# Optimization experiments

Measured on AMD Instinct MI355X. Metric: run time of the kernel, lower is better.

Reference implementation:

```python
import jax, jax.numpy as jnp
import numpy as np

N = 50000          # nodes
E = 800000         # edges (before self-loops)
G = 64             # graphs in batch
VOCAB = 10000
EMB = 62
HEADS = 4
C = 64             # per-head channels
NUM_CLASSES = 10
NEG_SLOPE = 0.2


def setup_inputs() -> dict:
    key = jax.random.key(0)
    ks = jax.random.split(key, 24)
    inp = {}
    inp['x_ids'] = jax.random.randint(ks[0], (N,), 0, VOCAB)
    inp['degrees'] = jax.random.uniform(ks[1], (N, 2), dtype=jnp.float32)
    inp['edge_src'] = jax.random.randint(ks[2], (E,), 0, N)
    inp['edge_dst'] = jax.random.randint(ks[3], (E,), 0, N)
    inp['batch'] = jnp.sort(jax.random.randint(ks[4], (N,), 0, G))
    # parameters
    inp['emb'] = jax.random.normal(ks[5], (VOCAB, EMB), dtype=jnp.float32)
    d_in = EMB + 2  # 64
    s = lambda f: 1.0 / np.sqrt(f)
    inp['W1'] = jax.random.normal(ks[6], (HEADS * C, d_in), dtype=jnp.float32) * s(d_in)
    inp['as1'] = jax.random.normal(ks[7], (HEADS, C), dtype=jnp.float32) * s(C)
    inp['ad1'] = jax.random.normal(ks[8], (HEADS, C), dtype=jnp.float32) * s(C)
    inp['b1'] = jnp.zeros((HEADS * C,), dtype=jnp.float32)
    inp['W2'] = jax.random.normal(ks[9], (HEADS * C, HEADS * C), dtype=jnp.float32) * s(HEADS * C)
    inp['as2'] = jax.random.normal(ks[10], (HEADS, C), dtype=jnp.float32) * s(C)
    inp['ad2'] = jax.random.normal(ks[11], (HEADS, C), dtype=jnp.float32) * s(C)
    inp['b2'] = jnp.zeros((HEADS * C,), dtype=jnp.float32)
    inp['W3'] = jax.random.normal(ks[12], (1 * C, HEADS * C), dtype=jnp.float32) * s(HEADS * C)
    inp['as3'] = jax.random.normal(ks[13], (1, C), dtype=jnp.float32) * s(C)
    inp['ad3'] = jax.random.normal(ks[14], (1, C), dtype=jnp.float32) * s(C)
    inp['b3'] = jnp.zeros((C,), dtype=jnp.float32)
    inp['linW'] = jax.random.normal(ks[15], (NUM_CLASSES, C), dtype=jnp.float32) * s(C)
    inp['linb'] = jnp.zeros((NUM_CLASSES,), dtype=jnp.float32)
    return inp


def gat_conv(x, src, dst, W, att_src, att_dst, bias, heads, out_ch, concat):
    n = x.shape[0]
    h = (x @ W.T).reshape(n, heads, out_ch)              # [N,H,C]
    a_src = jnp.sum(h * att_src, axis=-1)                # [N,H]
    a_dst = jnp.sum(h * att_dst, axis=-1)                # [N,H]
    e = jax.nn.leaky_relu(a_src[src] + a_dst[dst], NEG_SLOPE)  # [E,H]
    # segmented softmax over incoming edges of each dst node
    emax = jax.ops.segment_max(e, dst, num_segments=n)
    ex = jnp.exp(e - emax[dst])
    denom = jax.ops.segment_sum(ex, dst, num_segments=n)
    alpha = ex / (denom[dst] + 1e-16)                    # [E,H]
    msg = h[src] * alpha[:, :, None]                     # [E,H,C]
    out = jax.ops.segment_sum(msg, dst, num_segments=n)  # [N,H,C]
    out = out.reshape(n, heads * out_ch) if concat else out.mean(axis=1)
    return out + bias


def reference(x_ids, degrees, edge_src, edge_dst, batch, emb,
              W1, as1, ad1, b1, W2, as2, ad2, b2, W3, as3, ad3, b3, linW, linb):
    n = x_ids.shape[0]
    # add self-loops (PyG GATConv default)
    loop = jnp.arange(n)
    src = jnp.concatenate([edge_src, loop])
    dst = jnp.concatenate([edge_dst, loop])
    x = jnp.concatenate([emb[x_ids], degrees], axis=1)   # [N, EMB+2]
    x = jax.nn.relu(gat_conv(x, src, dst, W1, as1, ad1, b1, HEADS, C, True))
    x = jax.nn.relu(gat_conv(x, src, dst, W2, as2, ad2, b2, HEADS, C, True))
    x = jax.nn.relu(gat_conv(x, src, dst, W3, as3, ad3, b3, 1, C, False))
    # global mean pool over graphs
    sums = jax.ops.segment_sum(x, batch, num_segments=G)                    # [G,C]
    cnts = jax.ops.segment_sum(jnp.ones((n,), x.dtype), batch, num_segments=G)
    pooled = sums / jnp.maximum(cnts, 1.0)[:, None]
    return pooled @ linW.T + linb                         # [G, num_classes]
```

## Files before the change

### kernel.cpp

```cpp
#include <hip/hip_runtime.h>
#include <hip/hip_bf16.h>
#include <cstdint>

#define NEG_SLOPE 0.2f

typedef __bf16 bf16x8 __attribute__((ext_vector_type(8)));
typedef float  f32x4  __attribute__((ext_vector_type(4)));

__device__ __forceinline__ unsigned short f2bf(float f) {
    unsigned int u = __float_as_uint(f);
    u += 0x7fffu + ((u >> 16) & 1u);
    return (unsigned short)(u >> 16);
}
__device__ __forceinline__ float bf2f(unsigned short u) {
    return __uint_as_float((unsigned int)u << 16);
}
__device__ __forceinline__ void fma2(float2& a, float ex, unsigned int u) {
    a.x = fmaf(ex, __uint_as_float(u << 16),         a.x);
    a.y = fmaf(ex, __uint_as_float(u & 0xffff0000u), a.y);
}

__global__ void prep_kernel(const float* __restrict__ W1, int n1,
                            const float* __restrict__ W2, int n2,
                            const float* __restrict__ W3, int n3,
                            unsigned short* __restrict__ w1b, unsigned short* __restrict__ w2b,
                            unsigned short* __restrict__ w3b,
                            const int* __restrict__ ids, const float* __restrict__ degs,
                            const float* __restrict__ emb, unsigned short* __restrict__ x,
                            int* __restrict__ cnt, int* __restrict__ bucket,
                            int* __restrict__ n_over,
                            const int* __restrict__ batch, int* __restrict__ gcnt,
                            int Nn, int G, int bW, int bX)
{
    int b = blockIdx.x;
    if (b < bW) {
        int i = b * 256 + threadIdx.x;
        if (i < n1) w1b[i] = f2bf(W1[i]);
        int j = i - n1;
        if (j >= 0 && j < n2) w2b[j] = f2bf(W2[j]);
        int k = j - n2;
        if (k >= 0 && k < n3) w3b[k] = f2bf(W3[k]);
    } else if (b < bX) {
        int node = (b - bW) * 4 + (threadIdx.x >> 6);
        int lane = threadIdx.x & 63;
        if (node < Nn) {
            int id = ids[node];
            float v;
            if (lane < 62) v = emb[(size_t)id * 62 + lane];
            else           v = degs[node * 2 + (lane - 62)];
            x[(size_t)node * 64 + lane] = f2bf(v);
            if (lane == 0) {
                cnt[node] = 1;
                bucket[(size_t)node * 64] = node;
            }
        }
    } else {
        int g = threadIdx.x;
        if (g < G) {
            int lo0 = 0, hi = Nn;
            while (lo0 < hi) { int mid = (lo0 + hi) >> 1; if (batch[mid] < g) lo0 = mid + 1; else hi = mid; }
            int lo1 = lo0; hi = Nn;
            while (lo1 < hi) { int mid = (lo1 + hi) >> 1; if (batch[mid] < g + 1) lo1 = mid + 1; else hi = mid; }
            gcnt[g] = lo1 - lo0;
        }
        if (threadIdx.x == 255) *n_over = 0;
    }
}

__global__ void gemm_scatter(const unsigned short* __restrict__ X, const unsigned short* __restrict__ Wb,
                             unsigned short* __restrict__ Hout,
                             const float* __restrict__ aSrc, const float* __restrict__ aDst,
                             float* __restrict__ a_s, float* __restrict__ a_d,
                             int Nn, int K, int F, int gemmB,
                             const int* __restrict__ esrc, const int* __restrict__ edst,
                             int* __restrict__ cnt, int* __restrict__ bucket,
                             int* __restrict__ ovd, int* __restrict__ ovs, int* __restrict__ n_over,
                             int E0)
{
    if (blockIdx.x >= gemmB) {
        int base = (blockIdx.x - gemmB) * 1024 + threadIdx.x;
        int sv[4], dv[4], pv[4];
        bool ok[4];
#pragma unroll
        for (int k = 0; k < 4; ++k) {
            int e = base + k * 256;
            ok[k] = (e < E0);
            if (ok[k]) { sv[k] = esrc[e]; dv[k] = edst[e]; }
        }
#pragma unroll
        for (int k = 0; k < 4; ++k)
            if (ok[k]) pv[k] = atomicAdd(&cnt[dv[k]], 1);
#pragma unroll
        for (int k = 0; k < 4; ++k) {
            if (ok[k]) {
                if (pv[k] < 64) bucket[(size_t)dv[k] * 64 + pv[k]] = sv[k];
                else {
                    int o = atomicAdd(n_over, 1);
                    ovd[o] = dv[k]; ovs[o] = sv[k];
                }
            }
        }
        return;
    }

    int wid  = (blockIdx.x * blockDim.x + threadIdx.x) >> 6;
    int lane = threadIdx.x & 63;
    int mtiles = (Nn + 63) >> 6;
    int ftiles = F >> 6;
    if (wid >= mtiles * ftiles) return;
    int ft = wid % ftiles;
    int mt = wid / ftiles;
    int m0 = mt << 6, f0 = ft << 6;
    int r = lane & 15, g = lane >> 4, g4 = g << 2;

    const unsigned short* xrow[4];
#pragma unroll
    for (int ja = 0; ja < 4; ++ja) {
        int row = m0 + ja * 16 + r;
        if (row >= Nn) row = Nn - 1;
        xrow[ja] = X + (size_t)row * K + g * 8;
    }
    const unsigned short* wrow = Wb + (size_t)(f0 + r) * K + g * 8;
    const size_t wstep = (size_t)16 * K;

    f32x4 acc[4][4];
#pragma unroll
    for (int a = 0; a < 4; ++a)
#pragma unroll
        for (int b = 0; b < 4; ++b) acc[a][b] = f32x4{0.f, 0.f, 0.f, 0.f};

    for (int k0 = 0; k0 < K; k0 += 32) {
        bf16x8 av[4], bv[4];
#pragma unroll
        for (int ja = 0; ja < 4; ++ja) av[ja] = *reinterpret_cast<const bf16x8*>(xrow[ja] + k0);
#pragma unroll
        for (int jb = 0; jb < 4; ++jb) bv[jb] = *reinterpret_cast<const bf16x8*>(wrow + jb * wstep + k0);
#pragma unroll
        for (int ja = 0; ja < 4; ++ja)
#pragma unroll
            for (int jb = 0; jb < 4; ++jb)
                acc[ja][jb] = __builtin_amdgcn_mfma_f32_16x16x32_bf16(av[ja], bv[jb], acc[ja][jb], 0, 0, 0);
    }

#pragma unroll
    for (int ja = 0; ja < 4; ++ja)
#pragma unroll
        for (int q = 0; q < 4; ++q) {
            int row = m0 + ja * 16 + g4 + q;
            if (row < Nn) {
#pragma unroll
                for (int jb = 0; jb < 4; ++jb)
                    Hout[(size_t)row * F + f0 + jb * 16 + r] = f2bf(acc[ja][jb][q]);
            }
        }

    float ps[4][4], pd[4][4];
#pragma unroll
    for (int ja = 0; ja < 4; ++ja)
#pragma unroll
        for (int q = 0; q < 4; ++q) { ps[ja][q] = 0.f; pd[ja][q] = 0.f; }
#pragma unroll
    for (int jb = 0; jb < 4; ++jb) {
        float ws_ = aSrc[f0 + jb * 16 + r];
        float wd_ = aDst[f0 + jb * 16 + r];
#pragma unroll
        for (int ja = 0; ja < 4; ++ja)
#pragma unroll
            for (int q = 0; q < 4; ++q) {
                ps[ja][q] += acc[ja][jb][q] * ws_;
                pd[ja][q] += acc[ja][jb][q] * wd_;
            }
    }
#pragma unroll
    for (int off = 1; off < 16; off <<= 1)
#pragma unroll
        for (int ja = 0; ja < 4; ++ja)
#pragma unroll
            for (int q = 0; q < 4; ++q) {
                ps[ja][q] += __shfl_xor(ps[ja][q], off, 64);
                pd[ja][q] += __shfl_xor(pd[ja][q], off, 64);
            }
    if (r == 0) {
        int Hh = F >> 6;
#pragma unroll
        for (int ja = 0; ja < 4; ++ja)
#pragma unroll
            for (int q = 0; q < 4; ++q) {
                int n = m0 + ja * 16 + g4 + q;
                if (n < Nn) {
                    a_s[(size_t)n * Hh + ft] = ps[ja][q];
                    a_d[(size_t)n * Hh + ft] = pd[ja][q];
                }
            }
    }
}

__global__ void gemm_mfma(const unsigned short* __restrict__ X, const unsigned short* __restrict__ Wb,
                          unsigned short* __restrict__ Hout,
                          const float* __restrict__ aSrc, const float* __restrict__ aDst,
                          float* __restrict__ a_s, float* __restrict__ a_d,
                          int Nn, int K, int F)
{
    int wid  = (blockIdx.x * blockDim.x + threadIdx.x) >> 6;
    int lane = threadIdx.x & 63;
    int mtiles = (Nn + 63) >> 6;
    int ftiles = F >> 6;
    if (wid >= mtiles * ftiles) return;
    int ft = wid % ftiles;
    int mt = wid / ftiles;
    int m0 = mt << 6, f0 = ft << 6;
    int r = lane & 15, g = lane >> 4, g4 = g << 2;

    const unsigned short* xrow[4];
#pragma unroll
    for (int ja = 0; ja < 4; ++ja) {
        int row = m0 + ja * 16 + r;
        if (row >= Nn) row = Nn - 1;
        xrow[ja] = X + (size_t)row * K + g * 8;
    }
    const unsigned short* wrow = Wb + (size_t)(f0 + r) * K + g * 8;
    const size_t wstep = (size_t)16 * K;

    f32x4 acc[4][4];
#pragma unroll
    for (int a = 0; a < 4; ++a)
#pragma unroll
        for (int b = 0; b < 4; ++b) acc[a][b] = f32x4{0.f, 0.f, 0.f, 0.f};

    for (int k0 = 0; k0 < K; k0 += 32) {
        bf16x8 av[4], bv[4];
#pragma unroll
        for (int ja = 0; ja < 4; ++ja) av[ja] = *reinterpret_cast<const bf16x8*>(xrow[ja] + k0);
#pragma unroll
        for (int jb = 0; jb < 4; ++jb) bv[jb] = *reinterpret_cast<const bf16x8*>(wrow + jb * wstep + k0);
#pragma unroll
        for (int ja = 0; ja < 4; ++ja)
#pragma unroll
            for (int jb = 0; jb < 4; ++jb)
                acc[ja][jb] = __builtin_amdgcn_mfma_f32_16x16x32_bf16(av[ja], bv[jb], acc[ja][jb], 0, 0, 0);
    }

#pragma unroll
    for (int ja = 0; ja < 4; ++ja)
#pragma unroll
        for (int q = 0; q < 4; ++q) {
            int row = m0 + ja * 16 + g4 + q;
            if (row < Nn) {
#pragma unroll
                for (int jb = 0; jb < 4; ++jb)
                    Hout[(size_t)row * F + f0 + jb * 16 + r] = f2bf(acc[ja][jb][q]);
            }
        }

    float ps[4][4], pd[4][4];
#pragma unroll
    for (int ja = 0; ja < 4; ++ja)
#pragma unroll
        for (int q = 0; q < 4; ++q) { ps[ja][q] = 0.f; pd[ja][q] = 0.f; }
#pragma unroll
    for (int jb = 0; jb < 4; ++jb) {
        float ws_ = aSrc[f0 + jb * 16 + r];
        float wd_ = aDst[f0 + jb * 16 + r];
#pragma unroll
        for (int ja = 0; ja < 4; ++ja)
#pragma unroll
            for (int q = 0; q < 4; ++q) {
                ps[ja][q] += acc[ja][jb][q] * ws_;
                pd[ja][q] += acc[ja][jb][q] * wd_;
            }
    }
#pragma unroll
    for (int off = 1; off < 16; off <<= 1)
#pragma unroll
        for (int ja = 0; ja < 4; ++ja)
#pragma unroll
            for (int q = 0; q < 4; ++q) {
                ps[ja][q] += __shfl_xor(ps[ja][q], off, 64);
                pd[ja][q] += __shfl_xor(pd[ja][q], off, 64);
            }
    if (r == 0) {
        int Hh = F >> 6;
#pragma unroll
        for (int ja = 0; ja < 4; ++ja)
#pragma unroll
            for (int q = 0; q < 4; ++q) {
                int n = m0 + ja * 16 + g4 + q;
                if (n < Nn) {
                    a_s[(size_t)n * Hh + ft] = ps[ja][q];
                    a_d[(size_t)n * Hh + ft] = pd[ja][q];
                }
            }
    }
}

template<int H>
__global__ void aggregate_kernel(const unsigned short* __restrict__ Hb,
                                 const float* __restrict__ a_s, const float* __restrict__ a_d,
                                 const int* __restrict__ cnt, const int* __restrict__ bucket,
                                 const int* __restrict__ ovd, const int* __restrict__ ovs,
                                 const int* __restrict__ n_over,
                                 const float* __restrict__ bias,
                                 unsigned short* __restrict__ out, int Nn)
{
    constexpr int F = H * 64;
    constexpr int VEC = F / 64;
    __shared__ uint2 s_pk[4][64][H];
    int w = threadIdx.x >> 6;
    int node = blockIdx.x * 4 + w;
    int lane = threadIdx.x & 63;
    if (node >= Nn) return;
    int deg = cnt[node];

    float adn[H];
#pragma unroll
    for (int h = 0; h < H; ++h) adn[h] = a_d[(size_t)node * H + h];

    if (deg <= 64) {
        bool act = lane < deg;
        int sn = act ? bucket[(size_t)node * 64 + lane] : 0;
        float v[H];
        if (H == 4) {
            const f32x4 av = *reinterpret_cast<const f32x4*>(a_s + (size_t)sn * 4);
#pragma unroll
            for (int h = 0; h < 4; ++h) {
                float t = av[h] + adn[h];
                t = (t > 0.f) ? t : NEG_SLOPE * t;
                v[h] = act ? t : -1e30f;
            }
        } else {
            float t = a_s[sn] + adn[0];
            t = (t > 0.f) ? t : NEG_SLOPE * t;
            v[0] = act ? t : -1e30f;
        }
        float m[H], e[H], s[H];
#pragma unroll
        for (int h = 0; h < H; ++h) {
            m[h] = v[h];
#pragma unroll
            for (int off = 32; off >= 1; off >>= 1)
                m[h] = fmaxf(m[h], __shfl_xor(m[h], off, 64));
        }
#pragma unroll
        for (int h = 0; h < H; ++h) {
            e[h] = act ? __expf(v[h] - m[h]) : 0.f;
            s[h] = e[h];
#pragma unroll
            for (int off = 32; off >= 1; off >>= 1)
                s[h] += __shfl_xor(s[h], off, 64);
        }

#pragma unroll
        for (int h = 0; h < H; ++h)
            s_pk[w][lane][h] = make_uint2((unsigned int)sn, __float_as_uint(e[h]));
        asm volatile("s_waitcnt lgkmcnt(0)" ::: "memory");

        if (H == 4) {
            int laneq = lane & 15, qtr = lane >> 4, hd = laneq >> 2;
            float2 acc2[8];
#pragma unroll
            for (int k = 0; k < 8; ++k) acc2[k] = make_float2(0.f, 0.f);
            int j = 0;
            for (; j + 8 <= deg; j += 8) {
                uint2 pkA = s_pk[w][j + qtr][hd];
                uint2 pkB = s_pk[w][j + 4 + qtr][hd];
                const uint4* hpA = reinterpret_cast<const uint4*>(Hb + (size_t)pkA.x * 256 + laneq * 16);
                const uint4* hpB = reinterpret_cast<const uint4*>(Hb + (size_t)pkB.x * 256 + laneq * 16);
                uint4 a0 = hpA[0];
                uint4 a1 = hpA[1];
                uint4 b0 = hpB[0];
                uint4 b1 = hpB[1];
                float exA = __uint_as_float(pkA.y);
                float exB = __uint_as_float(pkB.y);
                fma2(acc2[0], exA, a0.x); fma2(acc2[1], exA, a0.y);
                fma2(acc2[2], exA, a0.z); fma2(acc2[3], exA, a0.w);
                fma2(acc2[4], exA, a1.x); fma2(acc2[5], exA, a1.y);
                fma2(acc2[6], exA, a1.z); fma2(acc2[7], exA, a1.w);
                fma2(acc2[0], exB, b0.x); fma2(acc2[1], exB, b0.y);
                fma2(acc2[2], exB, b0.z); fma2(acc2[3], exB, b0.w);
                fma2(acc2[4], exB, b1.x); fma2(acc2[5], exB, b1.y);
                fma2(acc2[6], exB, b1.z); fma2(acc2[7], exB, b1.w);
            }
            for (; j < deg; j += 4) {
                uint2 pk = s_pk[w][j + qtr][hd];
                float ex = __uint_as_float(pk.y);
                const uint4* hp = reinterpret_cast<const uint4*>(Hb + (size_t)pk.x * 256 + laneq * 16);
                uint4 u0 = hp[0];
                uint4 u1 = hp[1];
                fma2(acc2[0], ex, u0.x); fma2(acc2[1], ex, u0.y);
                fma2(acc2[2], ex, u0.z); fma2(acc2[3], ex, u0.w);
                fma2(acc2[4], ex, u1.x); fma2(acc2[5], ex, u1.y);
                fma2(acc2[6], ex, u1.z); fma2(acc2[7], ex, u1.w);
            }
#pragma unroll
            for (int k = 0; k < 8; ++k) {
                acc2[k].x += __shfl_xor(acc2[k].x, 32, 64);
                acc2[k].y += __shfl_xor(acc2[k].y, 32, 64);
                acc2[k].x += __shfl_xor(acc2[k].x, 16, 64);
                acc2[k].y += __shfl_xor(acc2[k].y, 16, 64);
            }
            if (lane < 16) {
                int hd2 = lane >> 2;
                float sh = (hd2 == 0) ? s[0] : (hd2 == 1) ? s[1] : (hd2 == 2) ? s[2] : s[3];
                float inv = 1.f / (sh + 1e-16f);
                unsigned int pk8[8];
#pragma unroll
                for (int k = 0; k < 8; ++k) {
                    float t0 = acc2[k].x * inv + bias[lane * 16 + 2 * k];
                    float t1 = acc2[k].y * inv + bias[lane * 16 + 2 * k + 1];
                    unsigned int lo = f2bf(t0 > 0.f ? t0 : 0.f);
                    unsigned int hi = f2bf(t1 > 0.f ? t1 : 0.f);
                    pk8[k] = lo | (hi << 16);
                }
                uint4* op = reinterpret_cast<uint4*>(out + (size_t)node * 256 + lane * 16);
                op[0] = make_uint4(pk8[0], pk8[1], pk8[2], pk8[3]);
                op[1] = make_uint4(pk8[4], pk8[5], pk8[6], pk8[7]);
            }
        } else {
            int laneo = lane & 7, oct = lane >> 3;
            float2 acc2[4];
#pragma unroll
            for (int k = 0; k < 4; ++k) acc2[k] = make_float2(0.f, 0.f);
            int j = 0;
            for (; j + 16 <= deg; j += 16) {
                uint2 pkA = s_pk[w][j + oct][0];
                uint2 pkB = s_pk[w][j + 8 + oct][0];
                const uint4 a = *reinterpret_cast<const uint4*>(Hb + (size_t)pkA.x * 64 + laneo * 8);
                const uint4 b = *reinterpret_cast<const uint4*>(Hb + (size_t)pkB.x * 64 + laneo * 8);
                float exA = __uint_as_float(pkA.y);
                float exB = __uint_as_float(pkB.y);
                fma2(acc2[0], exA, a.x); fma2(acc2[1], exA, a.y);
                fma2(acc2[2], exA, a.z); fma2(acc2[3], exA, a.w);
                fma2(acc2[0], exB, b.x); fma2(acc2[1], exB, b.y);
                fma2(acc2[2], exB, b.z); fma2(acc2[3], exB, b.w);
            }
            for (; j < deg; j += 8) {
                uint2 pk = s_pk[w][j + oct][0];
                float ex = __uint_as_float(pk.y);
                const uint4 u = *reinterpret_cast<const uint4*>(Hb + (size_t)pk.x * 64 + laneo * 8);
                fma2(acc2[0], ex, u.x); fma2(acc2[1], ex, u.y);
                fma2(acc2[2], ex, u.z); fma2(acc2[3], ex, u.w);
            }
#pragma unroll
            for (int k = 0; k < 4; ++k) {
                acc2[k].x += __shfl_xor(acc2[k].x, 32, 64);
                acc2[k].y += __shfl_xor(acc2[k].y, 32, 64);
                acc2[k].x += __shfl_xor(acc2[k].x, 16, 64);
                acc2[k].y += __shfl_xor(acc2[k].y, 16, 64);
                acc2[k].x += __shfl_xor(acc2[k].x, 8, 64);
                acc2[k].y += __shfl_xor(acc2[k].y, 8, 64);
            }
            if (lane < 8) {
                float inv = 1.f / (s[0] + 1e-16f);
                unsigned int pk4[4];
#pragma unroll
                for (int k = 0; k < 4; ++k) {
                    float t0 = acc2[k].x * inv + bias[lane * 8 + 2 * k];
                    float t1 = acc2[k].y * inv + bias[lane * 8 + 2 * k + 1];
                    unsigned int lo = f2bf(t0 > 0.f ? t0 : 0.f);
                    unsigned int hi = f2bf(t1 > 0.f ? t1 : 0.f);
                    pk4[k] = lo | (hi << 16);
                }
                *reinterpret_cast<uint4*>(out + (size_t)node * 64 + lane * 8) =
                    make_uint4(pk4[0], pk4[1], pk4[2], pk4[3]);
            }
        }
        return;
    }

    int nov = *n_over;
    int head = (H == 1) ? 0 : (lane >> 4);
    float m[H], s[H];
#pragma unroll
    for (int h = 0; h < H; ++h) { m[h] = -1e30f; s[h] = 0.f; }
    {
        int sn = bucket[(size_t)node * 64 + lane];
#pragma unroll
        for (int h = 0; h < H; ++h) {
            float t = a_s[(size_t)sn * H + h] + adn[h];
            t = (t > 0.f) ? t : NEG_SLOPE * t;
            m[h] = fmaxf(m[h], t);
        }
    }
    for (int i = lane; i < nov; i += 64) {
        if (ovd[i] != node) continue;
        int sn = ovs[i];
#pragma unroll
        for (int h = 0; h < H; ++h) {
            float t = a_s[(size_t)sn * H + h] + adn[h];
            t = (t > 0.f) ? t : NEG_SLOPE * t;
            m[h] = fmaxf(m[h], t);
        }
    }
#pragma unroll
    for (int off = 32; off >= 1; off >>= 1)
#pragma unroll
        for (int h = 0; h < H; ++h) m[h] = fmaxf(m[h], __shfl_xor(m[h], off, 64));
    {
        int sn = bucket[(size_t)node * 64 + lane];
#pragma unroll
        for (int h = 0; h < H; ++h) {
            float t = a_s[(size_t)sn * H + h] + adn[h];
            t = (t > 0.f) ? t : NEG_SLOPE * t;
            s[h] += __expf(t - m[h]);
        }
    }
    for (int i = lane; i < nov; i += 64) {
        if (ovd[i] != node) continue;
        int sn = ovs[i];
#pragma unroll
        for (int h = 0; h < H; ++h) {
            float t = a_s[(size_t)sn * H + h] + adn[h];
            t = (t > 0.f) ? t : NEG_SLOPE * t;
            s[h] += __expf(t - m[h]);
        }
    }
#pragma unroll
    for (int off = 32; off >= 1; off >>= 1)
#pragma unroll
        for (int h = 0; h < H; ++h) s[h] += __shfl_xor(s[h], off, 64);

    float mh, sh, adh;
    if (H == 1) { mh = m[0]; sh = s[0]; adh = adn[0]; }
    else {
        mh  = (head == 0) ? m[0]   : (head == 1) ? m[1]   : (head == 2) ? m[2]   : m[3];
        sh  = (head == 0) ? s[0]   : (head == 1) ? s[1]   : (head == 2) ? s[2]   : s[3];
        adh = (head == 0) ? adn[0] : (head == 1) ? adn[1] : (head == 2) ? adn[2] : adn[3];
    }
    float inv = 1.f / (sh + 1e-16f);
    float acc[VEC];
#pragma unroll
    for (int k = 0; k < VEC; ++k) acc[k] = 0.f;
    for (int j = 0; j < 64; ++j) {
        int sn = bucket[(size_t)node * 64 + j];
        float t = a_s[(size_t)sn * H + head] + adh;
        t = (t > 0.f) ? t : NEG_SLOPE * t;
        float ex = __expf(t - mh);
        const unsigned short* hp = Hb + (size_t)sn * F + lane * VEC;
#pragma unroll
        for (int k = 0; k < VEC; ++k) acc[k] += ex * bf2f(hp[k]);
    }
    for (int i = 0; i < nov; ++i) {
        if (ovd[i] != node) continue;
        int sn = ovs[i];
        float t = a_s[(size_t)sn * H + head] + adh;
        t = (t > 0.f) ? t : NEG_SLOPE * t;
        float ex = __expf(t - mh);
        const unsigned short* hp = Hb + (size_t)sn * F + lane * VEC;
#pragma unroll
        for (int k = 0; k < VEC; ++k) acc[k] += ex * bf2f(hp[k]);
    }
#pragma unroll
    for (int k = 0; k < VEC; ++k) {
        int f = lane * VEC + k;
        float t = acc[k] * inv + bias[f];
        out[(size_t)node * F + f] = f2bf(t > 0.f ? t : 0.f);
    }
}

__global__ void pool_kernel(const unsigned short* __restrict__ x, const int* __restrict__ batch,
                            float* __restrict__ gsums, int Nn)
{
    int lane = threadIdx.x;
    int n0 = blockIdx.x * 64;
    if (n0 >= Nn) return;
    int nend = min(n0 + 64, Nn);
    float acc = 0.f;
    int gcur = batch[n0];
    for (int n = n0; n < nend; ++n) {
        int g = batch[n];
        if (g != gcur) {
            atomicAdd(&gsums[gcur * 64 + lane], acc);
            acc = 0.f;
            gcur = g;
        }
        acc += bf2f(x[(size_t)n * 64 + lane]);
    }
    atomicAdd(&gsums[gcur * 64 + lane], acc);
}

__global__ void final_kernel(const float* __restrict__ gsums, const int* __restrict__ gcnt,
                             const float* __restrict__ linW, const float* __restrict__ linb,
                             float* __restrict__ out, int G)
{
    int t = threadIdx.x;
    if (t >= G * 10) return;
    int g = t / 10, j = t % 10;
    float cnt = (float)max(gcnt[g], 1);
    float acc = 0.f;
#pragma unroll
    for (int c = 0; c < 64; ++c) acc += gsums[g * 64 + c] * linW[j * 64 + c];
    out[g * 10 + j] = acc / cnt + linb[j];
}

extern "C" void kernel_launch(void* const* d_in, const int* in_sizes, int n_in,
                              void* d_out, int out_size, void* d_ws, size_t ws_size,
                              hipStream_t stream)
{
    const int*   x_ids    = (const int*)d_in[0];
    const float* degrees  = (const float*)d_in[1];
    const int*   edge_src = (const int*)d_in[2];
    const int*   edge_dst = (const int*)d_in[3];
    const int*   batch    = (const int*)d_in[4];
    const float* emb      = (const float*)d_in[5];
    const float* W1  = (const float*)d_in[6];
    const float* as1 = (const float*)d_in[7];
    const float* ad1 = (const float*)d_in[8];
    const float* b1  = (const float*)d_in[9];
    const float* W2  = (const float*)d_in[10];
    const float* as2 = (const float*)d_in[11];
    const float* ad2 = (const float*)d_in[12];
    const float* b2  = (const float*)d_in[13];
    const float* W3  = (const float*)d_in[14];
    const float* as3 = (const float*)d_in[15];
    const float* ad3 = (const float*)d_in[16];
    const float* b3  = (const float*)d_in[17];
    const float* linW = (const float*)d_in[18];
    const float* linb = (const float*)d_in[19];

    const int N  = in_sizes[0];
    const int E0 = in_sizes[2];
    const int E2 = E0 + N;
    const int G  = out_size / 10;
    const int nW1 = in_sizes[6], nW2 = in_sizes[10], nW3 = in_sizes[14];

    char* p = (char*)d_ws;
    size_t off = 0;
    auto take = [&](size_t bytes) {
        void* q = p + off;
        off = (off + bytes + 255) & ~(size_t)255;
        return q;
    };
    unsigned short* xA  = (unsigned short*)take((size_t)N * 256 * 2);
    unsigned short* xB  = (unsigned short*)take((size_t)N * 256 * 2);
    float* a_s     = (float*)take((size_t)N * 4 * 4);
    float* a_d     = (float*)take((size_t)N * 4 * 4);
    int*   cnt     = (int*)take((size_t)(N + 64) * 4);
    int*   n_over  = cnt + N;
    int*   bucket  = (int*)take((size_t)N * 64 * 4);
    int*   ovd     = (int*)take((size_t)E2 * 4);
    int*   ovs     = (int*)take((size_t)E2 * 4);
    float* gsums   = (float*)take((size_t)G * 64 * 4);
    int*   gcnt    = (int*)take((size_t)G * 4);
    unsigned short* w1b = (unsigned short*)take((size_t)nW1 * 2);
    unsigned short* w2b = (unsigned short*)take((size_t)nW2 * 2);
    unsigned short* w3b = (unsigned short*)take((size_t)nW3 * 2);

    hipMemsetAsync(gsums, 0, (size_t)G * 64 * 4, stream);

    const int nodeBlocks4 = (N + 3) / 4;

    const int nWtot = nW1 + nW2 + nW3;
    const int bW = (nWtot + 255) / 256;
    const int bX = bW + nodeBlocks4;
    prep_kernel<<<bX + 1, 256, 0, stream>>>(W1, nW1, W2, nW2, W3, nW3, w1b, w2b, w3b,
                                            x_ids, degrees, emb, xA,
                                            cnt, bucket, n_over, batch, gcnt,
                                            N, G, bW, bX);

    const int mtiles = (N + 63) / 64;
    auto gemmBlocks = [&](int ftiles) { return (mtiles * ftiles + 3) / 4; };

    const int gemmB1   = gemmBlocks(4);
    const int scatterB = (E0 + 1023) / 1024;
    gemm_scatter<<<gemmB1 + scatterB, 256, 0, stream>>>(xA, w1b, xB, as1, ad1, a_s, a_d,
                                                        N, 64, 256, gemmB1,
                                                        edge_src, edge_dst, cnt, bucket,
                                                        ovd, ovs, n_over, E0);
    aggregate_kernel<4><<<nodeBlocks4, 256, 0, stream>>>(xB, a_s, a_d, cnt, bucket, ovd, ovs, n_over, b1, xA, N);
    gemm_mfma<<<gemmBlocks(4), 256, 0, stream>>>(xA, w2b, xB, as2, ad2, a_s, a_d, N, 256, 256);
    aggregate_kernel<4><<<nodeBlocks4, 256, 0, stream>>>(xB, a_s, a_d, cnt, bucket, ovd, ovs, n_over, b2, xA, N);
    gemm_mfma<<<gemmBlocks(1), 256, 0, stream>>>(xA, w3b, xB, as3, ad3, a_s, a_d, N, 256, 64);
    aggregate_kernel<1><<<nodeBlocks4, 256, 0, stream>>>(xB, a_s, a_d, cnt, bucket, ovd, ovs, n_over, b3, xA, N);

    pool_kernel<<<(N + 63) / 64, 64, 0, stream>>>(xA, batch, gsums, N);
    final_kernel<<<1, ((G * 10 + 63) / 64) * 64, 0, stream>>>(gsums, gcnt, linW, linb, (float*)d_out, G);
}
```

Before: 328.3 us.

## Split 4-head aggregation into per-head blocks mapped to XCDs

Adds a new aggregation kernel for the 4-head layers where each block handles one head for four nodes. Block indices are arranged so that each pair of XCDs serves a single head, which shrinks the working set of H features each XCD's L2 has to cache. The existing templated kernel is reduced to its single-head path. In exchange, the neighbour list, the softmax logits and the bucket reads are repeated once per head, and each gathered load is narrower (8 bytes instead of 32).

```diff
diff --git a/kernel.cpp b/kernel.cpp
--- a/kernel.cpp
+++ b/kernel.cpp
@@ -293,6 +293,141 @@
     }
 }
 
+__global__ void aggregate4_hs(const unsigned short* __restrict__ Hb,
+                              const float* __restrict__ a_s, const float* __restrict__ a_d,
+                              const int* __restrict__ cnt, const int* __restrict__ bucket,
+                              const int* __restrict__ ovd, const int* __restrict__ ovs,
+                              const int* __restrict__ n_over,
+                              const float* __restrict__ bias,
+                              unsigned short* __restrict__ out, int Nn)
+{
+    __shared__ uint2 s_pk[4][64];
+    int b = blockIdx.x;
+    int xcd = b & 7, slot = b >> 3;
+    int head = xcd >> 1;
+    int nb = slot * 2 + (xcd & 1);
+    int w = threadIdx.x >> 6;
+    int node = nb * 4 + w;
+    int lane = threadIdx.x & 63;
+    if (node >= Nn) return;
+    int deg = cnt[node];
+    float adh = a_d[(size_t)node * 4 + head];
+
+    if (deg <= 64) {
+        bool act = lane < deg;
+        int sn = act ? bucket[(size_t)node * 64 + lane] : 0;
+        float t = a_s[(size_t)sn * 4 + head] + adh;
+        t = (t > 0.f) ? t : NEG_SLOPE * t;
+        float v = act ? t : -1e30f;
+        float m = v;
+#pragma unroll
+        for (int off = 32; off >= 1; off >>= 1)
+            m = fmaxf(m, __shfl_xor(m, off, 64));
+        float e = act ? __expf(v - m) : 0.f;
+        float s = e;
+#pragma unroll
+        for (int off = 32; off >= 1; off >>= 1)
+            s += __shfl_xor(s, off, 64);
+
+        s_pk[w][lane] = make_uint2((unsigned int)sn, __float_as_uint(e));
+        asm volatile("s_waitcnt lgkmcnt(0)" ::: "memory");
+
+        int laneq = lane & 15, qtr = lane >> 4;
+        float2 acc2[2];
+        acc2[0] = make_float2(0.f, 0.f);
+        acc2[1] = make_float2(0.f, 0.f);
+        int j = 0;
+        for (; j + 8 <= deg; j += 8) {
+            uint2 pkA = s_pk[w][j + qtr];
+            uint2 pkB = s_pk[w][j + 4 + qtr];
+            const uint2 a = *reinterpret_cast<const uint2*>(Hb + (size_t)pkA.x * 256 + head * 64 + laneq * 4);
+            const uint2 bb = *reinterpret_cast<const uint2*>(Hb + (size_t)pkB.x * 256 + head * 64 + laneq * 4);
+            float exA = __uint_as_float(pkA.y);
+            float exB = __uint_as_float(pkB.y);
+            fma2(acc2[0], exA, a.x);  fma2(acc2[1], exA, a.y);
+            fma2(acc2[0], exB, bb.x); fma2(acc2[1], exB, bb.y);
+        }
+        for (; j < deg; j += 4) {
+            uint2 pk = s_pk[w][j + qtr];
+            float ex = __uint_as_float(pk.y);
+            const uint2 u = *reinterpret_cast<const uint2*>(Hb + (size_t)pk.x * 256 + head * 64 + laneq * 4);
+            fma2(acc2[0], ex, u.x); fma2(acc2[1], ex, u.y);
+        }
+#pragma unroll
+        for (int k = 0; k < 2; ++k) {
+            acc2[k].x += __shfl_xor(acc2[k].x, 32, 64);
+            acc2[k].y += __shfl_xor(acc2[k].y, 32, 64);
+            acc2[k].x += __shfl_xor(acc2[k].x, 16, 64);
+            acc2[k].y += __shfl_xor(acc2[k].y, 16, 64);
+        }
+        if (lane < 16) {
+            float inv = 1.f / (s + 1e-16f);
+            int fb = head * 64 + lane * 4;
+            float t0 = acc2[0].x * inv + bias[fb + 0];
+            float t1 = acc2[0].y * inv + bias[fb + 1];
+            float t2 = acc2[1].x * inv + bias[fb + 2];
+            float t3 = acc2[1].y * inv + bias[fb + 3];
+            unsigned int p0 = (unsigned int)f2bf(t0 > 0.f ? t0 : 0.f) |
+                              ((unsigned int)f2bf(t1 > 0.f ? t1 : 0.f) << 16);
+            unsigned int p1 = (unsigned int)f2bf(t2 > 0.f ? t2 : 0.f) |
+                              ((unsigned int)f2bf(t3 > 0.f ? t3 : 0.f) << 16);
+            *reinterpret_cast<uint2*>(out + (size_t)node * 256 + fb) = make_uint2(p0, p1);
+        }
+        return;
+    }
+
+    int nov = *n_over;
+    float m = -1e30f, s = 0.f;
+    {
+        int sn = bucket[(size_t)node * 64 + lane];
+        float t = a_s[(size_t)sn * 4 + head] + adh;
+        t = (t > 0.f) ? t : NEG_SLOPE * t;
+        m = t;
+    }
+    for (int i = lane; i < nov; i += 64) {
+        if (ovd[i] != node) continue;
+        float t = a_s[(size_t)ovs[i] * 4 + head] + adh;
+        t = (t > 0.f) ? t : NEG_SLOPE * t;
+        m = fmaxf(m, t);
+    }
+#pragma unroll
+    for (int off = 32; off >= 1; off >>= 1) m = fmaxf(m, __shfl_xor(m, off, 64));
+    {
+        int sn = bucket[(size_t)node * 64 + lane];
+        float t = a_s[(size_t)sn * 4 + head] + adh;
+        t = (t > 0.f) ? t : NEG_SLOPE * t;
+        s += __expf(t - m);
+    }
+    for (int i = lane; i < nov; i += 64) {
+        if (ovd[i] != node) continue;
+        float t = a_s[(size_t)ovs[i] * 4 + head] + adh;
+        t = (t > 0.f) ? t : NEG_SLOPE * t;
+        s += __expf(t - m);
+    }
+#pragma unroll
+    for (int off = 32; off >= 1; off >>= 1) s += __shfl_xor(s, off, 64);
+    float inv = 1.f / (s + 1e-16f);
+
+    float acc = 0.f;
+    for (int j = 0; j < 64; ++j) {
+        int sn = bucket[(size_t)node * 64 + j];
+        float t = a_s[(size_t)sn * 4 + head] + adh;
+        t = (t > 0.f) ? t : NEG_SLOPE * t;
+        float ex = __expf(t - m);
+        acc += ex * bf2f(Hb[(size_t)sn * 256 + head * 64 + lane]);
+    }
+    for (int i = 0; i < nov; ++i) {
+        if (ovd[i] != node) continue;
+        int sn = ovs[i];
+        float t = a_s[(size_t)sn * 4 + head] + adh;
+        t = (t > 0.f) ? t : NEG_SLOPE * t;
+        float ex = __expf(t - m);
+        acc += ex * bf2f(Hb[(size_t)sn * 256 + head * 64 + lane]);
+    }
+    float t = acc * inv + bias[head * 64 + lane];
+    out[(size_t)node * 256 + head * 64 + lane] = f2bf(t > 0.f ? t : 0.f);
+}
+
 template<int H>
 __global__ void aggregate_kernel(const unsigned short* __restrict__ Hb,
                                  const float* __restrict__ a_s, const float* __restrict__ a_d,
@@ -319,15 +454,7 @@
         bool act = lane < deg;
         int sn = act ? bucket[(size_t)node * 64 + lane] : 0;
         float v[H];
-        if (H == 4) {
-            const f32x4 av = *reinterpret_cast<const f32x4*>(a_s + (size_t)sn * 4);
-#pragma unroll
-            for (int h = 0; h < 4; ++h) {
-                float t = av[h] + adn[h];
-                t = (t > 0.f) ? t : NEG_SLOPE * t;
-                v[h] = act ? t : -1e30f;
-            }
-        } else {
+        {
             float t = a_s[sn] + adn[0];
             t = (t > 0.f) ? t : NEG_SLOPE * t;
             v[0] = act ? t : -1e30f;
@@ -354,178 +481,91 @@
             s_pk[w][lane][h] = make_uint2((unsigned int)sn, __float_as_uint(e[h]));
         asm volatile("s_waitcnt lgkmcnt(0)" ::: "memory");
 
-        if (H == 4) {
-            int laneq = lane & 15, qtr = lane >> 4, hd = laneq >> 2;
-            float2 acc2[8];
-#pragma unroll
-            for (int k = 0; k < 8; ++k) acc2[k] = make_float2(0.f, 0.f);
-            int j = 0;
-            for (; j + 8 <= deg; j += 8) {
-                uint2 pkA = s_pk[w][j + qtr][hd];
-                uint2 pkB = s_pk[w][j + 4 + qtr][hd];
-                const uint4* hpA = reinterpret_cast<const uint4*>(Hb + (size_t)pkA.x * 256 + laneq * 16);
-                const uint4* hpB = reinterpret_cast<const uint4*>(Hb + (size_t)pkB.x * 256 + laneq * 16);
-                uint4 a0 = hpA[0];
-                uint4 a1 = hpA[1];
-                uint4 b0 = hpB[0];
-                uint4 b1 = hpB[1];
-                float exA = __uint_as_float(pkA.y);
-                float exB = __uint_as_float(pkB.y);
-                fma2(acc2[0], exA, a0.x); fma2(acc2[1], exA, a0.y);
-                fma2(acc2[2], exA, a0.z); fma2(acc2[3], exA, a0.w);
-                fma2(acc2[4], exA, a1.x); fma2(acc2[5], exA, a1.y);
-                fma2(acc2[6], exA, a1.z); fma2(acc2[7], exA, a1.w);
-                fma2(acc2[0], exB, b0.x); fma2(acc2[1], exB, b0.y);
-                fma2(acc2[2], exB, b0.z); fma2(acc2[3], exB, b0.w);
-                fma2(acc2[4], exB, b1.x); fma2(acc2[5], exB, b1.y);
-                fma2(acc2[6], exB, b1.z); fma2(acc2[7], exB, b1.w);
-            }
-            for (; j < deg; j += 4) {
-                uint2 pk = s_pk[w][j + qtr][hd];
-                float ex = __uint_as_float(pk.y);
-                const uint4* hp = reinterpret_cast<const uint4*>(Hb + (size_t)pk.x * 256 + laneq * 16);
-                uint4 u0 = hp[0];
-                uint4 u1 = hp[1];
-                fma2(acc2[0], ex, u0.x); fma2(acc2[1], ex, u0.y);
-                fma2(acc2[2], ex, u0.z); fma2(acc2[3], ex, u0.w);
-                fma2(acc2[4], ex, u1.x); fma2(acc2[5], ex, u1.y);
-                fma2(acc2[6], ex, u1.z); fma2(acc2[7], ex, u1.w);
-            }
-#pragma unroll
-            for (int k = 0; k < 8; ++k) {
-                acc2[k].x += __shfl_xor(acc2[k].x, 32, 64);
-                acc2[k].y += __shfl_xor(acc2[k].y, 32, 64);
-                acc2[k].x += __shfl_xor(acc2[k].x, 16, 64);
-                acc2[k].y += __shfl_xor(acc2[k].y, 16, 64);
-            }
-            if (lane < 16) {
-                int hd2 = lane >> 2;
-                float sh = (hd2 == 0) ? s[0] : (hd2 == 1) ? s[1] : (hd2 == 2) ? s[2] : s[3];
-                float inv = 1.f / (sh + 1e-16f);
-                unsigned int pk8[8];
-#pragma unroll
-                for (int k = 0; k < 8; ++k) {
-                    float t0 = acc2[k].x * inv + bias[lane * 16 + 2 * k];
-                    float t1 = acc2[k].y * inv + bias[lane * 16 + 2 * k + 1];
-                    unsigned int lo = f2bf(t0 > 0.f ? t0 : 0.f);
-                    unsigned int hi = f2bf(t1 > 0.f ? t1 : 0.f);
-                    pk8[k] = lo | (hi << 16);
-                }
-                uint4* op = reinterpret_cast<uint4*>(out + (size_t)node * 256 + lane * 16);
-                op[0] = make_uint4(pk8[0], pk8[1], pk8[2], pk8[3]);
-                op[1] = make_uint4(pk8[4], pk8[5], pk8[6], pk8[7]);
-            }
-        } else {
-            int laneo = lane & 7, oct = lane >> 3;
-            float2 acc2[4];
-#pragma unroll
-            for (int k = 0; k < 4; ++k) acc2[k] = make_float2(0.f, 0.f);
-            int j = 0;
-            for (; j + 16 <= deg; j += 16) {
-                uint2 pkA = s_pk[w][j + oct][0];
-                uint2 pkB = s_pk[w][j + 8 + oct][0];
-                const uint4 a = *reinterpret_cast<const uint4*>(Hb + (size_t)pkA.x * 64 + laneo * 8);
-                const uint4 b = *reinterpret_cast<const uint4*>(Hb + (size_t)pkB.x * 64 + laneo * 8);
-                float exA = __uint_as_float(pkA.y);
-                float exB = __uint_as_float(pkB.y);
-                fma2(acc2[0], exA, a.x); fma2(acc2[1], exA, a.y);
-                fma2(acc2[2], exA, a.z); fma2(acc2[3], exA, a.w);
-                fma2(acc2[0], exB, b.x); fma2(acc2[1], exB, b.y);
-                fma2(acc2[2], exB, b.z); fma2(acc2[3], exB, b.w);
-            }
-            for (; j < deg; j += 8) {
-                uint2 pk = s_pk[w][j + oct][0];
-                float ex = __uint_as_float(pk.y);
-                const uint4 u = *reinterpret_cast<const uint4*>(Hb + (size_t)pk.x * 64 + laneo * 8);
-                fma2(acc2[0], ex, u.x); fma2(acc2[1], ex, u.y);
-                fma2(acc2[2], ex, u.z); fma2(acc2[3], ex, u.w);
-            }
+        int laneo = lane & 7, oct = lane >> 3;
+        float2 acc2[4];
+#pragma unroll
+        for (int k = 0; k < 4; ++k) acc2[k] = make_float2(0.f, 0.f);
+        int j = 0;
+        for (; j + 16 <= deg; j += 16) {
+            uint2 pkA = s_pk[w][j + oct][0];
+            uint2 pkB = s_pk[w][j + 8 + oct][0];
+            const uint4 a = *reinterpret_cast<const uint4*>(Hb + (size_t)pkA.x * 64 + laneo * 8);
+            const uint4 b = *reinterpret_cast<const uint4*>(Hb + (size_t)pkB.x * 64 + laneo * 8);
+            float exA = __uint_as_float(pkA.y);
+            float exB = __uint_as_float(pkB.y);
+            fma2(acc2[0], exA, a.x); fma2(acc2[1], exA, a.y);
+            fma2(acc2[2], exA, a.z); fma2(acc2[3], exA, a.w);
+            fma2(acc2[0], exB, b.x); fma2(acc2[1], exB, b.y);
+            fma2(acc2[2], exB, b.z); fma2(acc2[3], exB, b.w);
+        }
+        for (; j < deg; j += 8) {
+            uint2 pk = s_pk[w][j + oct][0];
+            float ex = __uint_as_float(pk.y);
+            const uint4 u = *reinterpret_cast<const uint4*>(Hb + (size_t)pk.x * 64 + laneo * 8);
+            fma2(acc2[0], ex, u.x); fma2(acc2[1], ex, u.y);
+            fma2(acc2[2], ex, u.z); fma2(acc2[3], ex, u.w);
+        }
+#pragma unroll
+        for (int k = 0; k < 4; ++k) {
+            acc2[k].x += __shfl_xor(acc2[k].x, 32, 64);
+            acc2[k].y += __shfl_xor(acc2[k].y, 32, 64);
+            acc2[k].x += __shfl_xor(acc2[k].x, 16, 64);
+            acc2[k].y += __shfl_xor(acc2[k].y, 16, 64);
+            acc2[k].x += __shfl_xor(acc2[k].x, 8, 64);
+            acc2[k].y += __shfl_xor(acc2[k].y, 8, 64);
+        }
+        if (lane < 8) {
+            float inv = 1.f / (s[0] + 1e-16f);
+            unsigned int pk4[4];
 #pragma unroll
             for (int k = 0; k < 4; ++k) {
-                acc2[k].x += __shfl_xor(acc2[k].x, 32, 64);
-                acc2[k].y += __shfl_xor(acc2[k].y, 32, 64);
-                acc2[k].x += __shfl_xor(acc2[k].x, 16, 64);
-                acc2[k].y += __shfl_xor(acc2[k].y, 16, 64);
-                acc2[k].x += __shfl_xor(acc2[k].x, 8, 64);
-                acc2[k].y += __shfl_xor(acc2[k].y, 8, 64);
-            }
-            if (lane < 8) {
-                float inv = 1.f / (s[0] + 1e-16f);
-                unsigned int pk4[4];
-#pragma unroll
-                for (int k = 0; k < 4; ++k) {
-                    float t0 = acc2[k].x * inv + bias[lane * 8 + 2 * k];
-                    float t1 = acc2[k].y * inv + bias[lane * 8 + 2 * k + 1];
-                    unsigned int lo = f2bf(t0 > 0.f ? t0 : 0.f);
-                    unsigned int hi = f2bf(t1 > 0.f ? t1 : 0.f);
-                    pk4[k] = lo | (hi << 16);
-                }
-                *reinterpret_cast<uint4*>(out + (size_t)node * 64 + lane * 8) =
-                    make_uint4(pk4[0], pk4[1], pk4[2], pk4[3]);
-            }
+                float t0 = acc2[k].x * inv + bias[lane * 8 + 2 * k];
+                float t1 = acc2[k].y * inv + bias[lane * 8 + 2 * k + 1];
+                unsigned int lo = f2bf(t0 > 0.f ? t0 : 0.f);
+                unsigned int hi = f2bf(t1 > 0.f ? t1 : 0.f);
+                pk4[k] = lo | (hi << 16);
+            }
+            *reinterpret_cast<uint4*>(out + (size_t)node * 64 + lane * 8) =
+                make_uint4(pk4[0], pk4[1], pk4[2], pk4[3]);
         }
         return;
     }
 
     int nov = *n_over;
-    int head = (H == 1) ? 0 : (lane >> 4);
+    int head = 0;
     float m[H], s[H];
 #pragma unroll
     for (int h = 0; h < H; ++h) { m[h] = -1e30f; s[h] = 0.f; }
     {
         int sn = bucket[(size_t)node * 64 + lane];
-#pragma unroll
-        for (int h = 0; h < H; ++h) {
-            float t = a_s[(size_t)sn * H + h] + adn[h];
-            t = (t > 0.f) ? t : NEG_SLOPE * t;
-            m[h] = fmaxf(m[h], t);
-        }
+        float t = a_s[(size_t)sn * H] + adn[0];
+        t = (t > 0.f) ? t : NEG_SLOPE * t;
+        m[0] = fmaxf(m[0], t);
     }
     for (int i = lane; i < nov; i += 64) {
         if (ovd[i] != node) continue;
-        int sn = ovs[i];
-#pragma unroll
-        for (int h = 0; h < H; ++h) {
-            float t = a_s[(size_t)sn * H + h] + adn[h];
-            t = (t > 0.f) ? t : NEG_SLOPE * t;
-            m[h] = fmaxf(m[h], t);
-        }
-    }
-#pragma unroll
-    for (int off = 32; off >= 1; off >>= 1)
-#pragma unroll
-        for (int h = 0; h < H; ++h) m[h] = fmaxf(m[h], __shfl_xor(m[h], off, 64));
+        float t = a_s[(size_t)ovs[i] * H] + adn[0];
+        t = (t > 0.f) ? t : NEG_SLOPE * t;
+        m[0] = fmaxf(m[0], t);
+    }
+#pragma unroll
+    for (int off = 32; off >= 1; off >>= 1) m[0] = fmaxf(m[0], __shfl_xor(m[0], off, 64));
     {
         int sn = bucket[(size_t)node * 64 + lane];
-#pragma unroll
-        for (int h = 0; h < H; ++h) {
-            float t = a_s[(size_t)sn * H + h] + adn[h];
-            t = (t > 0.f) ? t : NEG_SLOPE * t;
-            s[h] += __expf(t - m[h]);
-        }
+        float t = a_s[(size_t)sn * H] + adn[0];
+        t = (t > 0.f) ? t : NEG_SLOPE * t;
+        s[0] += __expf(t - m[0]);
     }
     for (int i = lane; i < nov; i += 64) {
         if (ovd[i] != node) continue;
-        int sn = ovs[i];
-#pragma unroll
-        for (int h = 0; h < H; ++h) {
-            float t = a_s[(size_t)sn * H + h] + adn[h];
-            t = (t > 0.f) ? t : NEG_SLOPE * t;
-            s[h] += __expf(t - m[h]);
-        }
-    }
-#pragma unroll
-    for (int off = 32; off >= 1; off >>= 1)
-#pragma unroll
-        for (int h = 0; h < H; ++h) s[h] += __shfl_xor(s[h], off, 64);
-
-    float mh, sh, adh;
-    if (H == 1) { mh = m[0]; sh = s[0]; adh = adn[0]; }
-    else {
-        mh  = (head == 0) ? m[0]   : (head == 1) ? m[1]   : (head == 2) ? m[2]   : m[3];
-        sh  = (head == 0) ? s[0]   : (head == 1) ? s[1]   : (head == 2) ? s[2]   : s[3];
-        adh = (head == 0) ? adn[0] : (head == 1) ? adn[1] : (head == 2) ? adn[2] : adn[3];
-    }
+        float t = a_s[(size_t)ovs[i] * H] + adn[0];
+        t = (t > 0.f) ? t : NEG_SLOPE * t;
+        s[0] += __expf(t - m[0]);
+    }
+#pragma unroll
+    for (int off = 32; off >= 1; off >>= 1) s[0] += __shfl_xor(s[0], off, 64);
+
+    float mh = m[0], sh = s[0], adh = adn[0];
     float inv = 1.f / (sh + 1e-16f);
     float acc[VEC];
 #pragma unroll
@@ -660,15 +700,17 @@
     const int mtiles = (N + 63) / 64;
     auto gemmBlocks = [&](int ftiles) { return (mtiles * ftiles + 3) / 4; };
 
+    const int hsBlocks = 8 * ((nodeBlocks4 + 1) / 2);
+
     const int gemmB1   = gemmBlocks(4);
     const int scatterB = (E0 + 1023) / 1024;
     gemm_scatter<<<gemmB1 + scatterB, 256, 0, stream>>>(xA, w1b, xB, as1, ad1, a_s, a_d,
                                                         N, 64, 256, gemmB1,
                                                         edge_src, edge_dst, cnt, bucket,
                                                         ovd, ovs, n_over, E0);
-    aggregate_kernel<4><<<nodeBlocks4, 256, 0, stream>>>(xB, a_s, a_d, cnt, bucket, ovd, ovs, n_over, b1, xA, N);
+    aggregate4_hs<<<hsBlocks, 256, 0, stream>>>(xB, a_s, a_d, cnt, bucket, ovd, ovs, n_over, b1, xA, N);
     gemm_mfma<<<gemmBlocks(4), 256, 0, stream>>>(xA, w2b, xB, as2, ad2, a_s, a_d, N, 256, 256);
-    aggregate_kernel<4><<<nodeBlocks4, 256, 0, stream>>>(xB, a_s, a_d, cnt, bucket, ovd, ovs, n_over, b2, xA, N);
+    aggregate4_hs<<<hsBlocks, 256, 0, stream>>>(xB, a_s, a_d, cnt, bucket, ovd, ovs, n_over, b2, xA, N);
     gemm_mfma<<<gemmBlocks(1), 256, 0, stream>>>(xA, w3b, xB, as3, ad3, a_s, a_d, N, 256, 64);
     aggregate_kernel<1><<<nodeBlocks4, 256, 0, stream>>>(xB, a_s, a_d, cnt, bucket, ovd, ovs, n_over, b3, xA, N);
 
```

Measured after the change: 386.6 us. 17.7% more time.
